# Kernel optimization log

Hardware: AMD Instinct MI355X
Metric: run time of the kernel (lower is better)

Reference implementation:

```python
import jax, jax.numpy as jnp
import numpy as np

B, C, W, H = 16, 512, 64, 64
D = 16  # linear out features


def setup_inputs() -> dict:
    key = jax.random.key(0)
    k1, k2, k3, k4, k5 = jax.random.split(key, 5)
    x = jax.random.normal(k1, (B, C, W, H), dtype=jnp.float32)
    # nn.LazyLinear(16) with in_features = W*H
    Wq = jax.random.normal(k2, (D, W * H), dtype=jnp.float32) * 0.02
    bq = jnp.zeros((D,), dtype=jnp.float32)
    Wk = jax.random.normal(k3, (D, W * H), dtype=jnp.float32) * 0.02
    bk = jnp.zeros((D,), dtype=jnp.float32)
    return {"x": x, "Wq": Wq, "bq": bq, "Wk": Wk, "bk": bk}


def reference(x, Wq, bq, Wk, bk):
    b, c, w, h = x.shape
    xf = x.reshape(b, c, w * h)                      # [B, C, W*H]
    q = jnp.einsum('bcs,ds->bcd', xf, Wq) + bq       # [B, C, 16]
    k = jnp.einsum('bcs,ds->bcd', xf, Wk) + bk       # [B, C, 16]
    kq = jnp.einsum('bcd,bed->bce', q, k)            # [B, C, C]
    # torch nn.Softmax2d applies softmax over dim -3; for the 3D tensor
    # [B, C, C] that is the batch axis (axis 0) -- faithful reproduction.
    A = jax.nn.softmax(kq, axis=0)                   # [B, C, C]
    # Per-sample 1x1 conv with weight[o, i] = A[b, i, o] (note the transpose
    # from the permute([3,2,1,0]) in the torch code).
    out = jnp.einsum('bio,biwh->bowh', A, x)         # [B, C, W, H]
    return out
```

## Files before the change

kernel.cpp:

```cpp
#include <hip/hip_runtime.h>
#include <hip/hip_bf16.h>
#include <stdint.h>

typedef __attribute__((ext_vector_type(8))) short short8;
typedef __attribute__((ext_vector_type(4))) float floatx4;

#define B_ 16
#define C_ 512
#define S_ 4096
#define D_ 16

__device__ __forceinline__ unsigned short f2bf(float f) {
    union { float f; unsigned int i; } v;
    v.f = f;
    unsigned int u = v.i;
    return (unsigned short)((u + 0x7FFFu + ((u >> 16) & 1u)) >> 16);
}
__device__ __forceinline__ unsigned int pack2bf(float lo, float hi) {
    __hip_bfloat162 h = __float22bfloat162_rn(make_float2(lo, hi));
    union { __hip_bfloat162 h; unsigned int u; } v;
    v.h = h;
    return v.u;
}
__device__ __forceinline__ short8 cvt8p(float4 a, float4 b) {
    union { unsigned int u[4]; short8 s; } r;
    r.u[0] = pack2bf(a.x, a.y);
    r.u[1] = pack2bf(a.z, a.w);
    r.u[2] = pack2bf(b.x, b.y);
    r.u[3] = pack2bf(b.z, b.w);
    return r.s;
}

__global__ __launch_bounds__(256) void qk_kernel(
    const float* __restrict__ x,
    const float* __restrict__ Wq,
    const float* __restrict__ bq,
    const float* __restrict__ Wk,
    const float* __restrict__ bk,
    float* __restrict__ qkp)
{
    int lane = threadIdx.x & 63;
    int w    = threadIdx.x >> 6;
    int gw   = blockIdx.x * 4 + w;
    int row_tile = gw >> 2;
    int ks       = gw & 3;
    int m  = lane & 15;
    int q8 = lane >> 4;
    int k0 = ks * 1024;

    const float* ax = x  + (size_t)(row_tile * 16 + m) * S_ + k0 + q8 * 8;
    const float* aq = Wq + (size_t)m * S_ + k0 + q8 * 8;
    const float* ak = Wk + (size_t)m * S_ + k0 + q8 * 8;

    floatx4 accq = {0.f, 0.f, 0.f, 0.f};
    floatx4 acck = {0.f, 0.f, 0.f, 0.f};
#pragma unroll 4
    for (int it = 0; it < 32; ++it) {
        float4 xa = *(const float4*)(ax + it * 32);
        float4 xb2 = *(const float4*)(ax + it * 32 + 4);
        float4 qa = *(const float4*)(aq + it * 32);
        float4 qb = *(const float4*)(aq + it * 32 + 4);
        float4 ka = *(const float4*)(ak + it * 32);
        float4 kb2 = *(const float4*)(ak + it * 32 + 4);
        short8 a   = cvt8p(xa, xb2);
        short8 bq8 = cvt8p(qa, qb);
        short8 bk8 = cvt8p(ka, kb2);
        accq = __builtin_amdgcn_mfma_f32_16x16x32_bf16(a, bq8, accq, 0, 0, 0);
        acck = __builtin_amdgcn_mfma_f32_16x16x32_bf16(a, bk8, acck, 0, 0, 0);
    }
    float biasq = (ks == 0) ? bq[m] : 0.f;
    float biask = (ks == 0) ? bk[m] : 0.f;
    float* outp = qkp + (size_t)ks * 8192 * 32;
#pragma unroll
    for (int r = 0; r < 4; ++r) {
        int row = row_tile * 16 + q8 * 4 + r;
        outp[(size_t)row * 32 + m]      = accq[r] + biasq;
        outp[(size_t)row * 32 + 16 + m] = acck[r] + biask;
    }
}

__global__ __launch_bounds__(256) void reduce_kernel(
    const float* __restrict__ qkp, float* __restrict__ qred)
{
    int g = blockIdx.x * 256 + threadIdx.x;
    const float4* p = (const float4*)qkp + g;
    float4 a = p[0], b = p[65536], c = p[131072], d = p[196608];
    float4 r;
    r.x = a.x + b.x + c.x + d.x;
    r.y = a.y + b.y + c.y + d.y;
    r.z = a.z + b.z + c.z + d.z;
    r.w = a.w + b.w + c.w + d.w;
    ((float4*)qred)[g] = r;
}

__global__ __launch_bounds__(512) void softmax_kernel(
    const float* __restrict__ qred,
    unsigned short* __restrict__ Abf)
{
    __shared__ float lq[B_][32][17];
    __shared__ float lk[B_][16][17];
    int i0 = blockIdx.x * 32;
    int o0 = blockIdx.y * 16;
    int tid = threadIdx.x;

    {
        int d = tid & 15, il = tid >> 4;
#pragma unroll
        for (int b = 0; b < 16; ++b)
            lq[b][il][d] = qred[(size_t)(b * C_ + i0 + il) * 32 + d];
    }
    if (tid < 256) {
        int d = tid & 15, ol = tid >> 4;
#pragma unroll
        for (int b = 0; b < 16; ++b)
            lk[b][ol][d] = qred[(size_t)(b * C_ + o0 + ol) * 32 + 16 + d];
    }
    __syncthreads();

    int i = tid & 31;
    int o = tid >> 5;
    float v[16];
#pragma unroll
    for (int b = 0; b < 16; ++b) {
        float s = 0.f;
#pragma unroll
        for (int d = 0; d < 16; ++d) s += lq[b][i][d] * lk[b][o][d];
        v[b] = s;
    }
    float mx = v[0];
#pragma unroll
    for (int b = 1; b < 16; ++b) mx = fmaxf(mx, v[b]);
    float sum = 0.f;
#pragma unroll
    for (int b = 0; b < 16; ++b) { v[b] = __expf(v[b] - mx); sum += v[b]; }
    float inv = 1.0f / sum;
#pragma unroll
    for (int b = 0; b < 16; ++b)
        Abf[(size_t)(b * C_ + o0 + o) * C_ + i0 + i] = f2bf(v[b] * inv);
}

#define WP 20

__global__ __launch_bounds__(256) void av_kernel(
    const unsigned short* __restrict__ Abf,
    const float* __restrict__ x,
    float* __restrict__ out)
{
    __shared__ unsigned int At[128 * WP];
    __shared__ unsigned int Xt[128 * WP];
    int b  = blockIdx.z;
    int o0 = blockIdx.y * 128;
    int s0 = blockIdx.x * 128;
    int tid  = threadIdx.x;
    int lane = tid & 63;
    int w    = tid >> 6;
    int wm = (w >> 1) * 64;
    int wn = (w & 1) * 64;
    int fm = lane & 15;
    int q8 = lane >> 4;

    floatx4 acc[4][4];
#pragma unroll
    for (int a = 0; a < 4; ++a)
#pragma unroll
        for (int c = 0; c < 4; ++c) acc[a][c] = (floatx4){0.f, 0.f, 0.f, 0.f};

    const unsigned short* Ab = Abf + (size_t)b * C_ * C_;
    const float* xb = x + (size_t)b * C_ * S_;

    int arow  = tid >> 1;
    int ahalf = tid & 1;
    int ip    = tid & 15;
    int sblk  = tid >> 4;

    for (int kb = 0; kb < 16; ++kb) {
        int i0 = kb * 32;
        {
            const uint4* src = (const uint4*)(Ab + (size_t)(o0 + arow) * C_ + i0 + ahalf * 16);
            uint4 v0 = src[0];
            uint4 v1 = src[1];
            *(uint4*)(&At[arow * WP + ahalf * 8])     = v0;
            *(uint4*)(&At[arow * WP + ahalf * 8 + 4]) = v1;
        }
        {
            const float* xr0 = xb + (size_t)(i0 + 2 * ip) * S_ + s0 + sblk * 8;
            const float* xr1 = xr0 + S_;
            float4 a0 = *(const float4*)(xr0);
            float4 a1 = *(const float4*)(xr0 + 4);
            float4 b0 = *(const float4*)(xr1);
            float4 b1 = *(const float4*)(xr1 + 4);
            unsigned int* dst = &Xt[(sblk * 8) * WP + ip];
            dst[0 * WP] = pack2bf(a0.x, b0.x);
            dst[1 * WP] = pack2bf(a0.y, b0.y);
            dst[2 * WP] = pack2bf(a0.z, b0.z);
            dst[3 * WP] = pack2bf(a0.w, b0.w);
            dst[4 * WP] = pack2bf(a1.x, b1.x);
            dst[5 * WP] = pack2bf(a1.y, b1.y);
            dst[6 * WP] = pack2bf(a1.z, b1.z);
            dst[7 * WP] = pack2bf(a1.w, b1.w);
        }
        __syncthreads();

        short8 af[4], bfr[4];
#pragma unroll
        for (int t = 0; t < 4; ++t)
            af[t] = *(const short8*)(&At[(wm + t * 16 + fm) * WP + q8 * 4]);
#pragma unroll
        for (int t = 0; t < 4; ++t)
            bfr[t] = *(const short8*)(&Xt[(wn + t * 16 + fm) * WP + q8 * 4]);
#pragma unroll
        for (int a = 0; a < 4; ++a)
#pragma unroll
            for (int c = 0; c < 4; ++c)
                acc[a][c] = __builtin_amdgcn_mfma_f32_16x16x32_bf16(af[a], bfr[c], acc[a][c], 0, 0, 0);
        __syncthreads();
    }

    float* ob = out + (size_t)b * C_ * S_;
#pragma unroll
    for (int a = 0; a < 4; ++a) {
        int orow = o0 + wm + a * 16 + q8 * 4;
#pragma unroll
        for (int c = 0; c < 4; ++c) {
            int sc = s0 + wn + c * 16 + fm;
#pragma unroll
            for (int r = 0; r < 4; ++r)
                ob[(size_t)(orow + r) * S_ + sc] = acc[a][c][r];
        }
    }
}

extern "C" void kernel_launch(void* const* d_in, const int* in_sizes, int n_in,
                              void* d_out, int out_size, void* d_ws, size_t ws_size,
                              hipStream_t stream) {
    const float* x  = (const float*)d_in[0];
    const float* Wq = (const float*)d_in[1];
    const float* bq = (const float*)d_in[2];
    const float* Wk = (const float*)d_in[3];
    const float* bk = (const float*)d_in[4];
    float* out = (float*)d_out;

    float* qkp = (float*)d_ws;
    float* qred = (float*)((char*)d_ws + (size_t)4 * 1024 * 1024);
    unsigned short* Abf =
        (unsigned short*)((char*)d_ws + (size_t)5 * 1024 * 1024);

    qk_kernel<<<512, 256, 0, stream>>>(x, Wq, bq, Wk, bk, qkp);
    reduce_kernel<<<256, 256, 0, stream>>>(qkp, qred);
    softmax_kernel<<<dim3(16, 32), 512, 0, stream>>>(qred, Abf);
    av_kernel<<<dim3(32, 4, 16), 256, 0, stream>>>(Abf, x, out);
}
```

Baseline: 342.4 us.

## Load A tiles via global_load_lds, widen AV k-step, split QK reduction eightfold

```diff
diff --git a/kernel.cpp b/kernel.cpp
--- a/kernel.cpp
+++ b/kernel.cpp
@@ -31,6 +31,13 @@
     return r.s;
 }
 
+__device__ __forceinline__ void gl16(const void* g, void* l) {
+    __builtin_amdgcn_global_load_lds(
+        (const __attribute__((address_space(1))) unsigned int*)g,
+        (__attribute__((address_space(3))) unsigned int*)l, 16, 0, 0);
+}
+
+template <int NS>
 __global__ __launch_bounds__(256) void qk_kernel(
     const float* __restrict__ x,
     const float* __restrict__ Wq,
@@ -42,11 +49,11 @@
     int lane = threadIdx.x & 63;
     int w    = threadIdx.x >> 6;
     int gw   = blockIdx.x * 4 + w;
-    int row_tile = gw >> 2;
-    int ks       = gw & 3;
+    int row_tile = gw / NS;
+    int ks       = gw % NS;
     int m  = lane & 15;
     int q8 = lane >> 4;
-    int k0 = ks * 1024;
+    int k0 = ks * (S_ / NS);
 
     const float* ax = x  + (size_t)(row_tile * 16 + m) * S_ + k0 + q8 * 8;
     const float* aq = Wq + (size_t)m * S_ + k0 + q8 * 8;
@@ -55,7 +62,7 @@
     floatx4 accq = {0.f, 0.f, 0.f, 0.f};
     floatx4 acck = {0.f, 0.f, 0.f, 0.f};
 #pragma unroll 4
-    for (int it = 0; it < 32; ++it) {
+    for (int it = 0; it < S_ / NS / 32; ++it) {
         float4 xa = *(const float4*)(ax + it * 32);
         float4 xb2 = *(const float4*)(ax + it * 32 + 4);
         float4 qa = *(const float4*)(aq + it * 32);
@@ -79,17 +86,18 @@
     }
 }
 
+template <int NS>
 __global__ __launch_bounds__(256) void reduce_kernel(
     const float* __restrict__ qkp, float* __restrict__ qred)
 {
     int g = blockIdx.x * 256 + threadIdx.x;
     const float4* p = (const float4*)qkp + g;
-    float4 a = p[0], b = p[65536], c = p[131072], d = p[196608];
-    float4 r;
-    r.x = a.x + b.x + c.x + d.x;
-    r.y = a.y + b.y + c.y + d.y;
-    r.z = a.z + b.z + c.z + d.z;
-    r.w = a.w + b.w + c.w + d.w;
+    float4 r = p[0];
+#pragma unroll
+    for (int k = 1; k < NS; ++k) {
+        float4 v = p[(size_t)k * 65536];
+        r.x += v.x; r.y += v.y; r.z += v.z; r.w += v.w;
+    }
     ((float4*)qred)[g] = r;
 }
 
@@ -139,15 +147,15 @@
         Abf[(size_t)(b * C_ + o0 + o) * C_ + i0 + i] = f2bf(v[b] * inv);
 }
 
-#define WP 20
+#define XP 36
 
 __global__ __launch_bounds__(256) void av_kernel(
     const unsigned short* __restrict__ Abf,
     const float* __restrict__ x,
     float* __restrict__ out)
 {
-    __shared__ unsigned int At[128 * WP];
-    __shared__ unsigned int Xt[128 * WP];
+    __shared__ unsigned int At[128 * 32];
+    __shared__ unsigned int Xt[128 * XP];
     int b  = blockIdx.z;
     int o0 = blockIdx.y * 128;
     int s0 = blockIdx.x * 128;
@@ -168,51 +176,50 @@
     const unsigned short* Ab = Abf + (size_t)b * C_ * C_;
     const float* xb = x + (size_t)b * C_ * S_;
 
-    int arow  = tid >> 1;
-    int ahalf = tid & 1;
-    int ip    = tid & 15;
-    int sblk  = tid >> 4;
-
-    for (int kb = 0; kb < 16; ++kb) {
-        int i0 = kb * 32;
-        {
-            const uint4* src = (const uint4*)(Ab + (size_t)(o0 + arow) * C_ + i0 + ahalf * 16);
-            uint4 v0 = src[0];
-            uint4 v1 = src[1];
-            *(uint4*)(&At[arow * WP + ahalf * 8])     = v0;
-            *(uint4*)(&At[arow * WP + ahalf * 8 + 4]) = v1;
-        }
-        {
-            const float* xr0 = xb + (size_t)(i0 + 2 * ip) * S_ + s0 + sblk * 8;
-            const float* xr1 = xr0 + S_;
-            float4 a0 = *(const float4*)(xr0);
-            float4 a1 = *(const float4*)(xr0 + 4);
-            float4 b0 = *(const float4*)(xr1);
-            float4 b1 = *(const float4*)(xr1 + 4);
-            unsigned int* dst = &Xt[(sblk * 8) * WP + ip];
-            dst[0 * WP] = pack2bf(a0.x, b0.x);
-            dst[1 * WP] = pack2bf(a0.y, b0.y);
-            dst[2 * WP] = pack2bf(a0.z, b0.z);
-            dst[3 * WP] = pack2bf(a0.w, b0.w);
-            dst[4 * WP] = pack2bf(a1.x, b1.x);
-            dst[5 * WP] = pack2bf(a1.y, b1.y);
-            dst[6 * WP] = pack2bf(a1.z, b1.z);
-            dst[7 * WP] = pack2bf(a1.w, b1.w);
+    int arow_l = (lane >> 3);
+    int acol   = (lane & 7) * 8;
+
+    int xc  = tid >> 3;
+    int xip = tid & 7;
+
+    for (int kb = 0; kb < 8; ++kb) {
+        int i0 = kb * 64;
+#pragma unroll
+        for (int q = 0; q < 4; ++q) {
+            const unsigned short* gp =
+                Ab + (size_t)(o0 + w * 32 + q * 8 + arow_l) * C_ + i0 + acol;
+            unsigned int* lp = At + (w * 32 + q * 8) * 32;
+            gl16(gp, lp);
+        }
+#pragma unroll
+        for (int r = 0; r < 4; ++r) {
+            int ip = r * 8 + xip;
+            const float* x0 = xb + (size_t)(i0 + 2 * ip) * S_ + s0 + xc * 4;
+            float4 va = *(const float4*)x0;
+            float4 vb = *(const float4*)(x0 + S_);
+            unsigned int* dst = &Xt[(xc * 4) * XP + ip];
+            dst[0 * XP] = pack2bf(va.x, vb.x);
+            dst[1 * XP] = pack2bf(va.y, vb.y);
+            dst[2 * XP] = pack2bf(va.z, vb.z);
+            dst[3 * XP] = pack2bf(va.w, vb.w);
         }
         __syncthreads();
 
-        short8 af[4], bfr[4];
-#pragma unroll
-        for (int t = 0; t < 4; ++t)
-            af[t] = *(const short8*)(&At[(wm + t * 16 + fm) * WP + q8 * 4]);
-#pragma unroll
-        for (int t = 0; t < 4; ++t)
-            bfr[t] = *(const short8*)(&Xt[(wn + t * 16 + fm) * WP + q8 * 4]);
-#pragma unroll
-        for (int a = 0; a < 4; ++a)
-#pragma unroll
-            for (int c = 0; c < 4; ++c)
-                acc[a][c] = __builtin_amdgcn_mfma_f32_16x16x32_bf16(af[a], bfr[c], acc[a][c], 0, 0, 0);
+#pragma unroll
+        for (int kc = 0; kc < 2; ++kc) {
+            short8 af[4], bfr[4];
+#pragma unroll
+            for (int t = 0; t < 4; ++t)
+                af[t] = *(const short8*)(&At[(wm + t * 16 + fm) * 32 + kc * 16 + q8 * 4]);
+#pragma unroll
+            for (int t = 0; t < 4; ++t)
+                bfr[t] = *(const short8*)(&Xt[(wn + t * 16 + fm) * XP + kc * 16 + q8 * 4]);
+#pragma unroll
+            for (int a = 0; a < 4; ++a)
+#pragma unroll
+                for (int c = 0; c < 4; ++c)
+                    acc[a][c] = __builtin_amdgcn_mfma_f32_16x16x32_bf16(af[a], bfr[c], acc[a][c], 0, 0, 0);
+        }
         __syncthreads();
     }
 
@@ -240,13 +247,23 @@
     const float* bk = (const float*)d_in[4];
     float* out = (float*)d_out;
 
-    float* qkp = (float*)d_ws;
-    float* qred = (float*)((char*)d_ws + (size_t)4 * 1024 * 1024);
-    unsigned short* Abf =
-        (unsigned short*)((char*)d_ws + (size_t)5 * 1024 * 1024);
-
-    qk_kernel<<<512, 256, 0, stream>>>(x, Wq, bq, Wk, bk, qkp);
-    reduce_kernel<<<256, 256, 0, stream>>>(qkp, qred);
-    softmax_kernel<<<dim3(16, 32), 512, 0, stream>>>(qred, Abf);
-    av_kernel<<<dim3(32, 4, 16), 256, 0, stream>>>(Abf, x, out);
-}
+    if (ws_size >= (size_t)17 * 1024 * 1024) {
+        float* qkp = (float*)d_ws;
+        float* qred = (float*)((char*)d_ws + (size_t)8 * 1024 * 1024);
+        unsigned short* Abf =
+            (unsigned short*)((char*)d_ws + (size_t)9 * 1024 * 1024);
+        qk_kernel<8><<<1024, 256, 0, stream>>>(x, Wq, bq, Wk, bk, qkp);
+        reduce_kernel<8><<<256, 256, 0, stream>>>(qkp, qred);
+        softmax_kernel<<<dim3(16, 32), 512, 0, stream>>>(qred, Abf);
+        av_kernel<<<dim3(32, 4, 16), 256, 0, stream>>>(Abf, x, out);
+    } else {
+        float* qkp = (float*)d_ws;
+        float* qred = (float*)((char*)d_ws + (size_t)4 * 1024 * 1024);
+        unsigned short* Abf =
+            (unsigned short*)((char*)d_ws + (size_t)5 * 1024 * 1024);
+        qk_kernel<4><<<512, 256, 0, stream>>>(x, Wq, bq, Wk, bk, qkp);
+        reduce_kernel<4><<<256, 256, 0, stream>>>(qkp, qred);
+        softmax_kernel<<<dim3(16, 32), 512, 0, stream>>>(qred, Abf);
+        av_kernel<<<dim3(32, 4, 16), 256, 0, stream>>>(Abf, x, out);
+    }
+}
```

Result: faster. 327.2 us (-4.5%).
